# Performance work log

Hardware: AMD Instinct MI355X
Metric: run time of the kernel (lower is better)

## Reference

```python
import jax, jax.numpy as jnp
import numpy as np

DECAY = 0.99
EPS = 1e-12  # torch F.normalize eps


def setup_inputs() -> dict:
    key = jax.random.key(0)
    ks = jax.random.split(key, 5)
    B, S, H, M = 4, 4096, 1024, 256
    x = jax.random.normal(ks[0], (B, S, H), dtype=jnp.float32)
    Wq = jax.random.normal(ks[1], (M, H), dtype=jnp.float32) * (H ** -0.5)
    Wk = jax.random.normal(ks[2], (M, H), dtype=jnp.float32) * (H ** -0.5)
    Wv = jax.random.normal(ks[3], (M, H), dtype=jnp.float32) * (H ** -0.5)
    # original inits W_out to zeros; use small random weights so the baseline output is non-trivial
    Wo = jax.random.normal(ks[4], (H, M), dtype=jnp.float32) * (M ** -0.5)
    M0 = jnp.zeros((M, M), dtype=jnp.float32)
    return {"x": x, "Wq": Wq, "Wk": Wk, "Wv": Wv, "Wo": Wo, "M0": M0, "chunk_size": 64}


def _l2norm(t):
    return t / jnp.maximum(jnp.linalg.norm(t, axis=-1, keepdims=True), EPS)


def reference(x, Wq, Wk, Wv, Wo, M0, chunk_size):
    B, S, H = x.shape
    m = Wq.shape[0]
    q = jnp.einsum('bsh,mh->bsm', x, Wq)
    k = _l2norm(jnp.einsum('bsh,mh->bsm', x, Wk))
    v = _l2norm(jnp.einsum('bsh,mh->bsm', x, Wv))
    n_chunks = S // chunk_size
    # (n_chunks, B, c, m)
    qc = q.reshape(B, n_chunks, chunk_size, m).transpose(1, 0, 2, 3)
    kc = k.reshape(B, n_chunks, chunk_size, m).transpose(1, 0, 2, 3)
    vc = v.reshape(B, n_chunks, chunk_size, m).transpose(1, 0, 2, 3)
    decay_c = DECAY ** chunk_size
    scale = 1.0 / (B * chunk_size)

    def step(M, qkv):
        qch, kch, vch = qkv
        r = jnp.einsum('bcm,nm->bcn', qch, M)  # q @ M.T
        outer = jnp.einsum('bci,bcj->ij', vch, kch) * scale
        return decay_c * M + outer, r

    _, rs = jax.lax.scan(step, M0, (qc, kc, vc))  # rs: (n_chunks, B, c, m)
    retrieved = rs.transpose(1, 0, 2, 3).reshape(B, S, m)
    return jnp.einsum('bsm,hm->bsh', retrieved, Wo)
```

## Files before the change

### kernel.cpp

```cpp
#include <hip/hip_runtime.h>
#include <math.h>

#define BB 4
#define SS 4096
#define HH 1024
#define MM 256
#define CHUNK 64
#define NCHUNK 64
#define ROWS (BB*SS)
#define QKV_LD 768
#define DECAY_F 0.99

typedef unsigned short u16;
typedef __attribute__((ext_vector_type(8))) short bf16x8;
typedef __attribute__((ext_vector_type(8))) unsigned short u16x8;
typedef __attribute__((ext_vector_type(4))) float f32x4;

__device__ inline u16 f2b(float f) {
  union { float f; unsigned u; } v; v.f = f;
  unsigned r = v.u + 0x7FFF + ((v.u >> 16) & 1);
  return (u16)(r >> 16);
}
__device__ inline float b2f(u16 h) {
  union { unsigned u; float f; } v; v.u = ((unsigned)h) << 16; return v.f;
}

__device__ inline void gload16(const void* g, void* l) {
  __builtin_amdgcn_global_load_lds(
      (const __attribute__((address_space(1))) unsigned int*)g,
      (__attribute__((address_space(3))) unsigned int*)l, 16, 0, 0);
}

__global__ __launch_bounds__(256) void cast_x_kernel(const float* __restrict__ src,
                                                     u16* __restrict__ dst) {
  int i = blockIdx.x * 256 + threadIdx.x;
  float4 v = reinterpret_cast<const float4*>(src)[i];
  ushort4 o;
  o.x = f2b(v.x); o.y = f2b(v.y); o.z = f2b(v.z); o.w = f2b(v.w);
  reinterpret_cast<ushort4*>(dst)[i] = o;
}

__global__ __launch_bounds__(256) void cast_w_kernel(const float* __restrict__ Wq,
                                                     const float* __restrict__ Wk,
                                                     const float* __restrict__ Wv,
                                                     const float* __restrict__ Wo,
                                                     u16* __restrict__ Wqkv_b,
                                                     u16* __restrict__ Wo_b) {
  int b = blockIdx.x, which = b >> 8;
  int i = ((b & 255) << 8) + threadIdx.x;
  const float* src = which == 0 ? Wq : which == 1 ? Wk : which == 2 ? Wv : Wo;
  u16* dst = which < 3 ? Wqkv_b + which * (MM * HH) : Wo_b;
  float4 v = reinterpret_cast<const float4*>(src)[i];
  ushort4 o;
  o.x = f2b(v.x); o.y = f2b(v.y); o.z = f2b(v.z); o.w = f2b(v.w);
  reinterpret_cast<ushort4*>(dst)[i] = o;
}

template<int OUT_BF16>
__global__ __launch_bounds__(512, 2) void gemm256(const u16* __restrict__ A,
                                                  const u16* __restrict__ B,
                                                  void* __restrict__ Cv,
                                                  int K, int lda, int ldb, int ldc) {
  __shared__ bf16x8 LA[2][2][16][64];
  __shared__ bf16x8 LB[2][2][16][64];
  const int tid = threadIdx.x, lane = tid & 63, wv = tid >> 6;
  const int wr = wv >> 2, wc = wv & 3;

  const int gx = gridDim.x;
  const int nwg = gx * gridDim.y;
  const int lin = blockIdx.y * gx + blockIdx.x;
  const int chunk = nwg >> 3;
  const int orig = (lin & 7) * chunk + (lin >> 3);
  const int bx = orig % gx, by = orig / gx;
  const int row0 = by * 256, col0 = bx * 256;
  const int NT = K >> 6;

  const int fr = lane & 15;
  const int kg = (lane >> 4) << 3;

  auto stageA = [&](int kt, int db_, int tile) {
    const u16* g = A + (size_t)(row0 + tile * 16 + fr) * (size_t)lda + kt * 64 + kg;
    gload16(g,      &LA[db_][0][tile][0]);
    gload16(g + 32, &LA[db_][1][tile][0]);
  };
  auto stageB = [&](int kt, int db_, int tile) {
    const u16* g = B + (size_t)(col0 + tile * 16 + fr) * (size_t)ldb + kt * 64 + kg;
    gload16(g,      &LB[db_][0][tile][0]);
    gload16(g + 32, &LB[db_][1][tile][0]);
  };

  bf16x8 aq[4][2], bq[4][2];
  auto readAquad = [&](int db_, int h) {
#pragma unroll
    for (int i = 0; i < 4; ++i)
#pragma unroll
      for (int s = 0; s < 2; ++s)
        aq[i][s] = LA[db_][s][wr * 8 + h * 4 + i][lane];
  };
  auto readBall = [&](int db_) {
#pragma unroll
    for (int n = 0; n < 4; ++n)
#pragma unroll
      for (int s = 0; s < 2; ++s)
        bq[n][s] = LB[db_][s][wc * 4 + n][lane];
  };

  f32x4 acc[8][4] = {};
  auto cluster = [&](int h, int nh) {
#pragma unroll
    for (int i = 0; i < 4; ++i)
#pragma unroll
      for (int j = 0; j < 2; ++j)
#pragma unroll
        for (int s = 0; s < 2; ++s)
          acc[h * 4 + i][nh * 2 + j] = __builtin_amdgcn_mfma_f32_16x16x32_bf16(
              aq[i][s], bq[nh * 2 + j][s], acc[h * 4 + i][nh * 2 + j], 0, 0, 0);
  };

  stageA(0, 0, wv); stageA(0, 0, wv + 8);
  stageB(0, 0, wv); stageB(0, 0, wv + 8);

  for (int kt = 0; kt < NT; ++kt) {
    const int db = kt & 1, sb = db ^ 1;
    asm volatile("s_waitcnt vmcnt(0)" ::: "memory");
    __builtin_amdgcn_s_barrier();
    asm volatile("" ::: "memory");
    if (kt + 1 < NT) {
      stageA(kt + 1, sb, wv); stageA(kt + 1, sb, wv + 8);
      stageB(kt + 1, sb, wv); stageB(kt + 1, sb, wv + 8);
    }
    readAquad(db, 0);
    readBall(db);
    __builtin_amdgcn_s_setprio(1);
    cluster(0, 0); cluster(0, 1);
    __builtin_amdgcn_s_setprio(0);
    readAquad(db, 1);
    __builtin_amdgcn_s_setprio(1);
    cluster(1, 0); cluster(1, 1);
    __builtin_amdgcn_s_setprio(0);
  }

  const int r4 = (lane >> 4) << 2;
  const int cc = lane & 15;
#pragma unroll
  for (int mi = 0; mi < 8; ++mi)
#pragma unroll
    for (int nj = 0; nj < 4; ++nj)
#pragma unroll
      for (int r = 0; r < 4; ++r) {
        int lr = wr * 128 + mi * 16 + r4 + r;
        int lc = wc * 64 + nj * 16 + cc;
        float vv = acc[mi][nj][r];
        if (OUT_BF16) ((u16*)Cv)[(size_t)(row0 + lr) * ldc + col0 + lc] = f2b(vv);
        else          ((float*)Cv)[(size_t)(row0 + lr) * ldc + col0 + lc] = vv;
      }
}

#define M_OUTER 2
#define M_RETR  3

template<int MODE>
__global__ __launch_bounds__(256) void gemm128(const u16* __restrict__ A,
                                               const u16* __restrict__ Bg,
                                               void* __restrict__ Cv,
                                               int K, int lda, int ldb,
                                               float scale) {
  __shared__ bf16x8 As[3][512];
  __shared__ bf16x8 Bs[3][512];
  const int tid = threadIdx.x, lane = tid & 63, wv = tid >> 6;
  const int wr = wv >> 1, wc = wv & 1;
  const int t = blockIdx.z;
  const int bx = blockIdx.x, by = blockIdx.y;
  const int row0 = by * 128;
  const int col0 = bx * 128;
  const int NK = K >> 5;
  const u16* Bbase = (MODE == M_RETR) ? (Bg + (size_t)t * (MM * MM)) : Bg;

  auto stage = [&](int ks, int buf) {
    int koff;
    if (MODE == M_OUTER) koff = ((ks >> 1) << 12) + t * CHUNK + ((ks & 1) << 5);
    else                 koff = ks << 5;
#pragma unroll
    for (int j = 0; j < 2; ++j) {
      int m = j * 4 + wv;
      int rf = m * 16 + (lane & 15);
      size_t arow;
      if (MODE == M_RETR)
        arow = (size_t)(2 * by + (rf >> 6)) * SS + (size_t)t * CHUNK + (rf & 63);
      else
        arow = (size_t)(row0 + rf);
      const u16* ga = A + arow * (size_t)lda + koff + ((lane >> 4) << 3);
      gload16(ga, &As[buf][m * 64]);
      const u16* gb = Bbase + (size_t)(col0 + rf) * ldb + koff + ((lane >> 4) << 3);
      gload16(gb, &Bs[buf][m * 64]);
    }
  };

  f32x4 acc[4][4] = {};
  stage(0, 0);
  stage(1, 1);
  int rb = 0, sb = 2;
  for (int ks = 0; ks < NK; ++ks) {
    if (ks + 1 < NK) asm volatile("s_waitcnt vmcnt(4)" ::: "memory");
    else             asm volatile("s_waitcnt vmcnt(0)" ::: "memory");
    __builtin_amdgcn_s_barrier();
    asm volatile("" ::: "memory");
    if (ks + 2 < NK) stage(ks + 2, sb);
    bf16x8 af[4], bfr[4];
#pragma unroll
    for (int m = 0; m < 4; ++m) af[m] = As[rb][(wr * 4 + m) * 64 + lane];
#pragma unroll
    for (int n = 0; n < 4; ++n) bfr[n] = Bs[rb][(wc * 4 + n) * 64 + lane];
#pragma unroll
    for (int m = 0; m < 4; ++m)
#pragma unroll
      for (int n = 0; n < 4; ++n)
        acc[m][n] = __builtin_amdgcn_mfma_f32_16x16x32_bf16(af[m], bfr[n], acc[m][n], 0, 0, 0);
    rb = (rb == 2) ? 0 : rb + 1;
    sb = (sb == 2) ? 0 : sb + 1;
  }

  const int r4 = (lane >> 4) << 2;
  const int cc = lane & 15;
#pragma unroll
  for (int m = 0; m < 4; ++m)
#pragma unroll
    for (int n = 0; n < 4; ++n)
#pragma unroll
      for (int r = 0; r < 4; ++r) {
        int lr = wr * 64 + m * 16 + r4 + r;
        int lc = wc * 64 + n * 16 + cc;
        float vv = acc[m][n][r];
        if (MODE == M_OUTER) {
          ((float*)Cv)[(size_t)t * (MM * MM) + (size_t)(row0 + lr) * MM + col0 + lc] = vv * scale;
        } else {
          size_t rowg = (size_t)(2 * by + (lr >> 6)) * SS + (size_t)t * CHUNK + (lr & 63);
          ((u16*)Cv)[rowg * MM + col0 + lc] = f2b(vv);
        }
      }
}

__global__ __launch_bounds__(256) void l2normT_kernel(const u16* __restrict__ qkv,
                                                      u16* __restrict__ kT,
                                                      u16* __restrict__ vT) {
  __shared__ u16 T[256][72];
  __shared__ float ps[64][4];
  __shared__ float inv[64];
  const int tid = threadIdx.x;
  const int q = tid >> 6, rl = tid & 63;
  const int row0 = blockIdx.x * 64;
#pragma unroll 1
  for (int seg = 0; seg < 2; ++seg) {
    u16* dstT = seg ? vT : kT;
    const int segbase = 256 + seg * 256;
    float ss = 0.f;
#pragma unroll
    for (int i = 0; i < 8; ++i) {
      u16x8 v = *reinterpret_cast<const u16x8*>(
          qkv + (size_t)(row0 + rl) * QKV_LD + segbase + q * 64 + i * 8);
#pragma unroll
      for (int e = 0; e < 8; ++e) {
        float f = b2f(v[e]);
        ss += f * f;
        T[q * 64 + i * 8 + e][rl] = v[e];
      }
    }
    ps[rl][q] = ss;
    __syncthreads();
    if (tid < 64) {
      float s = ps[tid][0] + ps[tid][1] + ps[tid][2] + ps[tid][3];
      inv[tid] = 1.0f / fmaxf(sqrtf(s), 1e-12f);
    }
    __syncthreads();
#pragma unroll
    for (int p = 0; p < 8; ++p) {
      int c = p * 32 + q * 8 + (rl >> 3);
      int r0 = (rl & 7) * 8;
      u16x8 val = *reinterpret_cast<const u16x8*>(&T[c][r0]);
      u16x8 o;
#pragma unroll
      for (int e = 0; e < 8; ++e) o[e] = f2b(b2f(val[e]) * inv[r0 + e]);
      *reinterpret_cast<u16x8*>(dstT + (size_t)c * ROWS + row0 + r0) = o;
    }
    __syncthreads();
  }
}

__global__ __launch_bounds__(256) void prefix_kernel(const float* __restrict__ outer,
                                                     const float* __restrict__ M0,
                                                     u16* __restrict__ Mprev_b,
                                                     float decay_c) {
  int ij = blockIdx.x * 256 + threadIdx.x;
  float run = M0[ij];
  float pre[8];
#pragma unroll
  for (int d = 0; d < 8; ++d) pre[d] = outer[(size_t)d * (MM * MM) + ij];
#pragma unroll 1
  for (int tb = 0; tb < NCHUNK; tb += 8) {
#pragma unroll
    for (int d = 0; d < 8; ++d) {
      int tc = tb + d;
      float o = pre[d];
      if (tb + 8 < NCHUNK) pre[d] = outer[(size_t)(tc + 8) * (MM * MM) + ij];
      Mprev_b[(size_t)tc * (MM * MM) + ij] = f2b(run);
      run = decay_c * run + o;
    }
  }
}

extern "C" void kernel_launch(void* const* d_in, const int* in_sizes, int n_in,
                              void* d_out, int out_size, void* d_ws, size_t ws_size,
                              hipStream_t stream) {
  const float* x  = (const float*)d_in[0];
  const float* Wq = (const float*)d_in[1];
  const float* Wk = (const float*)d_in[2];
  const float* Wv = (const float*)d_in[3];
  const float* Wo = (const float*)d_in[4];
  const float* M0 = (const float*)d_in[5];
  float* out = (float*)d_out;

  char* ws = (char*)d_ws;
  u16*   xb      = (u16*)(ws);
  u16*   qkv_b   = (u16*)(ws + 33554432);
  u16*   Wqkv_b  = (u16*)(ws + 58720256);
  u16*   Wo_b    = (u16*)(ws + 60293120);
  u16*   kT      = (u16*)(ws);
  u16*   vT      = (u16*)(ws + 8388608);
  float* outer   = (float*)(ws + 16777216);
  u16*   Mprev_b = (u16*)(ws);
  u16*   r_b     = (u16*)(ws + 8388608);

  const float scale   = 1.0f / (BB * CHUNK);
  const float decay_c = (float)pow(DECAY_F, (double)CHUNK);
  dim3 blk(256), blk512(512);

  cast_x_kernel<<<(ROWS * HH / 4) / 256, blk, 0, stream>>>(x, xb);
  cast_w_kernel<<<1024, blk, 0, stream>>>(Wq, Wk, Wv, Wo, Wqkv_b, Wo_b);
  gemm256<1><<<dim3(QKV_LD / 256, ROWS / 256), blk512, 0, stream>>>(
      xb, Wqkv_b, qkv_b, HH, HH, HH, QKV_LD);
  l2normT_kernel<<<ROWS / 64, blk, 0, stream>>>(qkv_b, kT, vT);
  gemm128<M_OUTER><<<dim3(2, 2, NCHUNK), blk, 0, stream>>>(
      vT, kT, outer, MM, ROWS, ROWS, scale);
  prefix_kernel<<<(MM * MM) / 256, blk, 0, stream>>>(outer, M0, Mprev_b, decay_c);
  gemm128<M_RETR><<<dim3(2, 2, NCHUNK), blk, 0, stream>>>(
      qkv_b, Mprev_b, r_b, MM, QKV_LD, MM, 0.f);
  gemm256<0><<<dim3(HH / 256, ROWS / 256), blk512, 0, stream>>>(
      r_b, Wo_b, out, MM, MM, MM, HH);
}
```

Baseline: 151.1 us.

## Retile QKV GEMM to 256x192 tiles and interleave global prefetch with MFMA clusters

The gemm256 kernel gains an NBT template parameter. The QKV projection now uses 256x192 tiles, giving a 4x64 grid of 256 workgroups instead of 3x64 (192), so it fills the GPU's compute units better. The main loop no longer issues all next-tile global loads in one burst after the barrier. The loads are now spread across the four MFMA clusters, with partial vmcnt waits and extra barriers between phases, so memory traffic overlaps compute. The extra barriers add synchronisation cost and the 12-fragment layout gives an uneven B-tile split across waves.

```diff
diff --git a/kernel.cpp b/kernel.cpp
--- a/kernel.cpp
+++ b/kernel.cpp
@@ -56,15 +56,17 @@
   reinterpret_cast<ushort4*>(dst)[i] = o;
 }
 
-template<int OUT_BF16>
+template<int NBT, int OUT_BF16>
 __global__ __launch_bounds__(512, 2) void gemm256(const u16* __restrict__ A,
                                                   const u16* __restrict__ B,
                                                   void* __restrict__ Cv,
                                                   int K, int lda, int ldb, int ldc) {
+  constexpr int NFR = NBT / 4;
   __shared__ bf16x8 LA[2][2][16][64];
-  __shared__ bf16x8 LB[2][2][16][64];
+  __shared__ bf16x8 LB[2][2][NBT][64];
   const int tid = threadIdx.x, lane = tid & 63, wv = tid >> 6;
   const int wr = wv >> 2, wc = wv & 3;
+  const int ph3tile = (NBT == 16) ? (wv + 8) : (8 + (wv & 3));
 
   const int gx = gridDim.x;
   const int nwg = gx * gridDim.y;
@@ -72,7 +74,7 @@
   const int chunk = nwg >> 3;
   const int orig = (lin & 7) * chunk + (lin >> 3);
   const int bx = orig % gx, by = orig / gx;
-  const int row0 = by * 256, col0 = bx * 256;
+  const int row0 = by * 256, col0 = bx * (NBT * 16);
   const int NT = K >> 6;
 
   const int fr = lane & 15;
@@ -89,7 +91,7 @@
     gload16(g + 32, &LB[db_][1][tile][0]);
   };
 
-  bf16x8 aq[4][2], bq[4][2];
+  bf16x8 aq[4][2], bq[NFR][2];
   auto readAquad = [&](int db_, int h) {
 #pragma unroll
     for (int i = 0; i < 4; ++i)
@@ -97,47 +99,57 @@
       for (int s = 0; s < 2; ++s)
         aq[i][s] = LA[db_][s][wr * 8 + h * 4 + i][lane];
   };
-  auto readBall = [&](int db_) {
-#pragma unroll
-    for (int n = 0; n < 4; ++n)
+  auto readBhalf = [&](int db_, int half) {
+    const int n0 = half ? 2 : 0, n1 = half ? NFR : 2;
+#pragma unroll
+    for (int n = n0; n < n1; ++n)
 #pragma unroll
       for (int s = 0; s < 2; ++s)
-        bq[n][s] = LB[db_][s][wc * 4 + n][lane];
-  };
-
-  f32x4 acc[8][4] = {};
-  auto cluster = [&](int h, int nh) {
+        bq[n][s] = LB[db_][s][wc * NFR + n][lane];
+  };
+
+  f32x4 acc[8][NFR] = {};
+  auto cluster = [&](int h, int half) {
+    const int n0 = half ? 2 : 0, n1 = half ? NFR : 2;
 #pragma unroll
     for (int i = 0; i < 4; ++i)
 #pragma unroll
-      for (int j = 0; j < 2; ++j)
+      for (int n = n0; n < n1; ++n)
 #pragma unroll
         for (int s = 0; s < 2; ++s)
-          acc[h * 4 + i][nh * 2 + j] = __builtin_amdgcn_mfma_f32_16x16x32_bf16(
-              aq[i][s], bq[nh * 2 + j][s], acc[h * 4 + i][nh * 2 + j], 0, 0, 0);
+          acc[h * 4 + i][n] = __builtin_amdgcn_mfma_f32_16x16x32_bf16(
+              aq[i][s], bq[n][s], acc[h * 4 + i][n], 0, 0, 0);
   };
 
   stageA(0, 0, wv); stageA(0, 0, wv + 8);
-  stageB(0, 0, wv); stageB(0, 0, wv + 8);
+  stageB(0, 0, wv); stageB(0, 0, ph3tile);
 
   for (int kt = 0; kt < NT; ++kt) {
     const int db = kt & 1, sb = db ^ 1;
-    asm volatile("s_waitcnt vmcnt(0)" ::: "memory");
+    const bool pf = (kt + 1 < NT);
+    if (pf) stageA(kt + 1, sb, wv);
+    if (pf) asm volatile("s_waitcnt vmcnt(2)" ::: "memory");
+    else    asm volatile("s_waitcnt vmcnt(0)" ::: "memory");
     __builtin_amdgcn_s_barrier();
     asm volatile("" ::: "memory");
-    if (kt + 1 < NT) {
-      stageA(kt + 1, sb, wv); stageA(kt + 1, sb, wv + 8);
-      stageB(kt + 1, sb, wv); stageB(kt + 1, sb, wv + 8);
-    }
     readAquad(db, 0);
-    readBall(db);
-    __builtin_amdgcn_s_setprio(1);
-    cluster(0, 0); cluster(0, 1);
-    __builtin_amdgcn_s_setprio(0);
+    readBhalf(db, 0);
+    __builtin_amdgcn_s_setprio(1); cluster(0, 0); __builtin_amdgcn_s_setprio(0);
+    __builtin_amdgcn_s_barrier();
+    readBhalf(db, 1);
+    if (pf) stageA(kt + 1, sb, wv + 8);
+    __builtin_amdgcn_s_barrier();
+    __builtin_amdgcn_s_setprio(1); cluster(0, 1); __builtin_amdgcn_s_setprio(0);
+    __builtin_amdgcn_s_barrier();
     readAquad(db, 1);
-    __builtin_amdgcn_s_setprio(1);
-    cluster(1, 0); cluster(1, 1);
-    __builtin_amdgcn_s_setprio(0);
+    if (pf) stageB(kt + 1, sb, wv);
+    __builtin_amdgcn_s_barrier();
+    __builtin_amdgcn_s_setprio(1); cluster(1, 0); __builtin_amdgcn_s_setprio(0);
+    __builtin_amdgcn_s_barrier();
+    if (pf) stageB(kt + 1, sb, ph3tile);
+    __builtin_amdgcn_s_barrier();
+    __builtin_amdgcn_s_setprio(1); cluster(1, 1); __builtin_amdgcn_s_setprio(0);
+    __builtin_amdgcn_s_barrier();
   }
 
   const int r4 = (lane >> 4) << 2;
@@ -145,11 +157,11 @@
 #pragma unroll
   for (int mi = 0; mi < 8; ++mi)
 #pragma unroll
-    for (int nj = 0; nj < 4; ++nj)
+    for (int nj = 0; nj < NFR; ++nj)
 #pragma unroll
       for (int r = 0; r < 4; ++r) {
         int lr = wr * 128 + mi * 16 + r4 + r;
-        int lc = wc * 64 + nj * 16 + cc;
+        int lc = wc * (NFR * 16) + nj * 16 + cc;
         float vv = acc[mi][nj][r];
         if (OUT_BF16) ((u16*)Cv)[(size_t)(row0 + lr) * ldc + col0 + lc] = f2b(vv);
         else          ((float*)Cv)[(size_t)(row0 + lr) * ldc + col0 + lc] = vv;
@@ -336,7 +348,7 @@
 
   cast_x_kernel<<<(ROWS * HH / 4) / 256, blk, 0, stream>>>(x, xb);
   cast_w_kernel<<<1024, blk, 0, stream>>>(Wq, Wk, Wv, Wo, Wqkv_b, Wo_b);
-  gemm256<1><<<dim3(QKV_LD / 256, ROWS / 256), blk512, 0, stream>>>(
+  gemm256<12, 1><<<dim3(4, 64), blk512, 0, stream>>>(
       xb, Wqkv_b, qkv_b, HH, HH, HH, QKV_LD);
   l2normT_kernel<<<ROWS / 64, blk, 0, stream>>>(qkv_b, kT, vT);
   gemm128<M_OUTER><<<dim3(2, 2, NCHUNK), blk, 0, stream>>>(
@@ -344,6 +356,6 @@
   prefix_kernel<<<(MM * MM) / 256, blk, 0, stream>>>(outer, M0, Mprev_b, decay_c);
   gemm128<M_RETR><<<dim3(2, 2, NCHUNK), blk, 0, stream>>>(
       qkv_b, Mprev_b, r_b, MM, QKV_LD, MM, 0.f);
-  gemm256<0><<<dim3(HH / 256, ROWS / 256), blk512, 0, stream>>>(
+  gemm256<16, 0><<<dim3(4, 64), blk512, 0, stream>>>(
       r_b, Wo_b, out, MM, MM, MM, HH);
 }
```

New measurement: 146.4 us. -3.2%, faster.

## Shrink chunk GEMM tiles to 64x64, split l2norm by segment, interleave gemm256 prefetch

Applied to the files above, without the earlier changes.

Replaces the 128x128-tile outer-product and retrieval GEMMs with 64x64 tiles, taking the grid from 256 to 1024 blocks so the device's CUs have more work to spread across. The l2norm/transpose kernel now handles k and v in separate blocks through a second grid dimension instead of looping over both. The large gemm256 main loop issues its next-tile global loads in pieces between MFMA clusters, with extra barriers, rather than all at once after the wait. The cost is less reuse per block and added barrier overhead in gemm256.

```diff
diff --git a/kernel.cpp b/kernel.cpp
--- a/kernel.cpp
+++ b/kernel.cpp
@@ -97,12 +97,12 @@
       for (int s = 0; s < 2; ++s)
         aq[i][s] = LA[db_][s][wr * 8 + h * 4 + i][lane];
   };
-  auto readBall = [&](int db_) {
-#pragma unroll
-    for (int n = 0; n < 4; ++n)
+  auto readB2 = [&](int db_, int nh) {
+#pragma unroll
+    for (int j = 0; j < 2; ++j)
 #pragma unroll
       for (int s = 0; s < 2; ++s)
-        bq[n][s] = LB[db_][s][wc * 4 + n][lane];
+        bq[nh * 2 + j][s] = LB[db_][s][wc * 4 + nh * 2 + j][lane];
   };
 
   f32x4 acc[8][4] = {};
@@ -122,22 +122,30 @@
 
   for (int kt = 0; kt < NT; ++kt) {
     const int db = kt & 1, sb = db ^ 1;
-    asm volatile("s_waitcnt vmcnt(0)" ::: "memory");
+    const bool pf = (kt + 1 < NT);
+    if (pf) stageA(kt + 1, sb, wv);
+    if (pf) asm volatile("s_waitcnt vmcnt(2)" ::: "memory");
+    else    asm volatile("s_waitcnt vmcnt(0)" ::: "memory");
     __builtin_amdgcn_s_barrier();
     asm volatile("" ::: "memory");
-    if (kt + 1 < NT) {
-      stageA(kt + 1, sb, wv); stageA(kt + 1, sb, wv + 8);
-      stageB(kt + 1, sb, wv); stageB(kt + 1, sb, wv + 8);
-    }
     readAquad(db, 0);
-    readBall(db);
-    __builtin_amdgcn_s_setprio(1);
-    cluster(0, 0); cluster(0, 1);
-    __builtin_amdgcn_s_setprio(0);
+    readB2(db, 0);
+    __builtin_amdgcn_s_setprio(1); cluster(0, 0); __builtin_amdgcn_s_setprio(0);
+    __builtin_amdgcn_s_barrier();
+    readB2(db, 1);
+    if (pf) stageA(kt + 1, sb, wv + 8);
+    __builtin_amdgcn_s_barrier();
+    __builtin_amdgcn_s_setprio(1); cluster(0, 1); __builtin_amdgcn_s_setprio(0);
+    __builtin_amdgcn_s_barrier();
     readAquad(db, 1);
-    __builtin_amdgcn_s_setprio(1);
-    cluster(1, 0); cluster(1, 1);
-    __builtin_amdgcn_s_setprio(0);
+    if (pf) stageB(kt + 1, sb, wv);
+    __builtin_amdgcn_s_barrier();
+    __builtin_amdgcn_s_setprio(1); cluster(1, 0); __builtin_amdgcn_s_setprio(0);
+    __builtin_amdgcn_s_barrier();
+    if (pf) stageB(kt + 1, sb, wv + 8);
+    __builtin_amdgcn_s_barrier();
+    __builtin_amdgcn_s_setprio(1); cluster(1, 1); __builtin_amdgcn_s_setprio(0);
+    __builtin_amdgcn_s_barrier();
   }
 
   const int r4 = (lane >> 4) << 2;
@@ -156,66 +164,57 @@
       }
 }
 
-#define M_OUTER 2
-#define M_RETR  3
+#define G64_OUTER 0
+#define G64_RETR  1
 
 template<int MODE>
-__global__ __launch_bounds__(256) void gemm128(const u16* __restrict__ A,
-                                               const u16* __restrict__ Bg,
-                                               void* __restrict__ Cv,
-                                               int K, int lda, int ldb,
-                                               float scale) {
-  __shared__ bf16x8 As[3][512];
-  __shared__ bf16x8 Bs[3][512];
+__global__ __launch_bounds__(256) void gemm64(const u16* __restrict__ A,
+                                              const u16* __restrict__ Bg,
+                                              void* __restrict__ Cv,
+                                              float scale) {
+  __shared__ bf16x8 As[3][4][64];
+  __shared__ bf16x8 Bs[3][4][64];
+  constexpr int NK = 8;
   const int tid = threadIdx.x, lane = tid & 63, wv = tid >> 6;
   const int wr = wv >> 1, wc = wv & 1;
   const int t = blockIdx.z;
-  const int bx = blockIdx.x, by = blockIdx.y;
-  const int row0 = by * 128;
-  const int col0 = bx * 128;
-  const int NK = K >> 5;
-  const u16* Bbase = (MODE == M_RETR) ? (Bg + (size_t)t * (MM * MM)) : Bg;
+  const int i0 = blockIdx.y * 64;
+  const int j0 = blockIdx.x * 64;
+  const u16* Bbase = (MODE == G64_RETR) ? (Bg + (size_t)t * (MM * MM)) : Bg;
+  const int fr = lane & 15, kg = (lane >> 4) << 3;
 
   auto stage = [&](int ks, int buf) {
-    int koff;
-    if (MODE == M_OUTER) koff = ((ks >> 1) << 12) + t * CHUNK + ((ks & 1) << 5);
-    else                 koff = ks << 5;
-#pragma unroll
-    for (int j = 0; j < 2; ++j) {
-      int m = j * 4 + wv;
-      int rf = m * 16 + (lane & 15);
-      size_t arow;
-      if (MODE == M_RETR)
-        arow = (size_t)(2 * by + (rf >> 6)) * SS + (size_t)t * CHUNK + (rf & 63);
-      else
-        arow = (size_t)(row0 + rf);
-      const u16* ga = A + arow * (size_t)lda + koff + ((lane >> 4) << 3);
-      gload16(ga, &As[buf][m * 64]);
-      const u16* gb = Bbase + (size_t)(col0 + rf) * ldb + koff + ((lane >> 4) << 3);
-      gload16(gb, &Bs[buf][m * 64]);
+    if (MODE == G64_OUTER) {
+      int koff = ((ks >> 1) << 12) + t * CHUNK + ((ks & 1) << 5);
+      gload16(A     + (size_t)(i0 + wv * 16 + fr) * ROWS + koff + kg, &As[buf][wv][0]);
+      gload16(Bbase + (size_t)(j0 + wv * 16 + fr) * ROWS + koff + kg, &Bs[buf][wv][0]);
+    } else {
+      size_t arow = (size_t)blockIdx.y * SS + (size_t)t * CHUNK + wv * 16 + fr;
+      gload16(A     + arow * QKV_LD + ks * 32 + kg,                    &As[buf][wv][0]);
+      gload16(Bbase + (size_t)(j0 + wv * 16 + fr) * MM + ks * 32 + kg, &Bs[buf][wv][0]);
     }
   };
 
-  f32x4 acc[4][4] = {};
+  f32x4 acc[2][2] = {};
   stage(0, 0);
   stage(1, 1);
   int rb = 0, sb = 2;
   for (int ks = 0; ks < NK; ++ks) {
-    if (ks + 1 < NK) asm volatile("s_waitcnt vmcnt(4)" ::: "memory");
+    if (ks + 1 < NK) asm volatile("s_waitcnt vmcnt(2)" ::: "memory");
     else             asm volatile("s_waitcnt vmcnt(0)" ::: "memory");
     __builtin_amdgcn_s_barrier();
     asm volatile("" ::: "memory");
     if (ks + 2 < NK) stage(ks + 2, sb);
-    bf16x8 af[4], bfr[4];
-#pragma unroll
-    for (int m = 0; m < 4; ++m) af[m] = As[rb][(wr * 4 + m) * 64 + lane];
-#pragma unroll
-    for (int n = 0; n < 4; ++n) bfr[n] = Bs[rb][(wc * 4 + n) * 64 + lane];
-#pragma unroll
-    for (int m = 0; m < 4; ++m)
-#pragma unroll
-      for (int n = 0; n < 4; ++n)
-        acc[m][n] = __builtin_amdgcn_mfma_f32_16x16x32_bf16(af[m], bfr[n], acc[m][n], 0, 0, 0);
+    bf16x8 af[2], bf[2];
+#pragma unroll
+    for (int m = 0; m < 2; ++m) af[m] = As[rb][wr * 2 + m][lane];
+#pragma unroll
+    for (int n = 0; n < 2; ++n) bf[n] = Bs[rb][wc * 2 + n][lane];
+#pragma unroll
+    for (int m = 0; m < 2; ++m)
+#pragma unroll
+      for (int n = 0; n < 2; ++n)
+        acc[m][n] = __builtin_amdgcn_mfma_f32_16x16x32_bf16(af[m], bf[n], acc[m][n], 0, 0, 0);
     rb = (rb == 2) ? 0 : rb + 1;
     sb = (sb == 2) ? 0 : sb + 1;
   }
@@ -223,19 +222,19 @@
   const int r4 = (lane >> 4) << 2;
   const int cc = lane & 15;
 #pragma unroll
-  for (int m = 0; m < 4; ++m)
-#pragma unroll
-    for (int n = 0; n < 4; ++n)
+  for (int m = 0; m < 2; ++m)
+#pragma unroll
+    for (int n = 0; n < 2; ++n)
 #pragma unroll
       for (int r = 0; r < 4; ++r) {
-        int lr = wr * 64 + m * 16 + r4 + r;
-        int lc = wc * 64 + n * 16 + cc;
+        int lr = wr * 32 + m * 16 + r4 + r;
+        int lc = wc * 32 + n * 16 + cc;
         float vv = acc[m][n][r];
-        if (MODE == M_OUTER) {
-          ((float*)Cv)[(size_t)t * (MM * MM) + (size_t)(row0 + lr) * MM + col0 + lc] = vv * scale;
+        if (MODE == G64_OUTER) {
+          ((float*)Cv)[(size_t)t * (MM * MM) + (size_t)(i0 + lr) * MM + j0 + lc] = vv * scale;
         } else {
-          size_t rowg = (size_t)(2 * by + (lr >> 6)) * SS + (size_t)t * CHUNK + (lr & 63);
-          ((u16*)Cv)[rowg * MM + col0 + lc] = f2b(vv);
+          size_t rowg = (size_t)blockIdx.y * SS + (size_t)t * CHUNK + lr;
+          ((u16*)Cv)[rowg * MM + j0 + lc] = f2b(vv);
         }
       }
 }
@@ -249,40 +248,37 @@
   const int tid = threadIdx.x;
   const int q = tid >> 6, rl = tid & 63;
   const int row0 = blockIdx.x * 64;
-#pragma unroll 1
-  for (int seg = 0; seg < 2; ++seg) {
-    u16* dstT = seg ? vT : kT;
-    const int segbase = 256 + seg * 256;
-    float ss = 0.f;
-#pragma unroll
-    for (int i = 0; i < 8; ++i) {
-      u16x8 v = *reinterpret_cast<const u16x8*>(
-          qkv + (size_t)(row0 + rl) * QKV_LD + segbase + q * 64 + i * 8);
-#pragma unroll
-      for (int e = 0; e < 8; ++e) {
-        float f = b2f(v[e]);
-        ss += f * f;
-        T[q * 64 + i * 8 + e][rl] = v[e];
-      }
+  const int seg = blockIdx.y;
+  u16* dstT = seg ? vT : kT;
+  const int segbase = 256 + seg * 256;
+  float ss = 0.f;
+#pragma unroll
+  for (int i = 0; i < 8; ++i) {
+    u16x8 v = *reinterpret_cast<const u16x8*>(
+        qkv + (size_t)(row0 + rl) * QKV_LD + segbase + q * 64 + i * 8);
+#pragma unroll
+    for (int e = 0; e < 8; ++e) {
+      float f = b2f(v[e]);
+      ss += f * f;
+      T[q * 64 + i * 8 + e][rl] = v[e];
     }
-    ps[rl][q] = ss;
-    __syncthreads();
-    if (tid < 64) {
-      float s = ps[tid][0] + ps[tid][1] + ps[tid][2] + ps[tid][3];
-      inv[tid] = 1.0f / fmaxf(sqrtf(s), 1e-12f);
-    }
-    __syncthreads();
-#pragma unroll
-    for (int p = 0; p < 8; ++p) {
-      int c = p * 32 + q * 8 + (rl >> 3);
-      int r0 = (rl & 7) * 8;
-      u16x8 val = *reinterpret_cast<const u16x8*>(&T[c][r0]);
-      u16x8 o;
-#pragma unroll
-      for (int e = 0; e < 8; ++e) o[e] = f2b(b2f(val[e]) * inv[r0 + e]);
-      *reinterpret_cast<u16x8*>(dstT + (size_t)c * ROWS + row0 + r0) = o;
-    }
-    __syncthreads();
+  }
+  ps[rl][q] = ss;
+  __syncthreads();
+  if (tid < 64) {
+    float s = ps[tid][0] + ps[tid][1] + ps[tid][2] + ps[tid][3];
+    inv[tid] = 1.0f / fmaxf(sqrtf(s), 1e-12f);
+  }
+  __syncthreads();
+#pragma unroll
+  for (int p = 0; p < 8; ++p) {
+    int c = p * 32 + q * 8 + (rl >> 3);
+    int r0 = (rl & 7) * 8;
+    u16x8 val = *reinterpret_cast<const u16x8*>(&T[c][r0]);
+    u16x8 o;
+#pragma unroll
+    for (int e = 0; e < 8; ++e) o[e] = f2b(b2f(val[e]) * inv[r0 + e]);
+    *reinterpret_cast<u16x8*>(dstT + (size_t)c * ROWS + row0 + r0) = o;
   }
 }
 
@@ -338,12 +334,12 @@
   cast_w_kernel<<<1024, blk, 0, stream>>>(Wq, Wk, Wv, Wo, Wqkv_b, Wo_b);
   gemm256<1><<<dim3(QKV_LD / 256, ROWS / 256), blk512, 0, stream>>>(
       xb, Wqkv_b, qkv_b, HH, HH, HH, QKV_LD);
-  l2normT_kernel<<<ROWS / 64, blk, 0, stream>>>(qkv_b, kT, vT);
-  gemm128<M_OUTER><<<dim3(2, 2, NCHUNK), blk, 0, stream>>>(
-      vT, kT, outer, MM, ROWS, ROWS, scale);
+  l2normT_kernel<<<dim3(ROWS / 64, 2), blk, 0, stream>>>(qkv_b, kT, vT);
+  gemm64<G64_OUTER><<<dim3(4, 4, NCHUNK), blk, 0, stream>>>(
+      vT, kT, outer, scale);
   prefix_kernel<<<(MM * MM) / 256, blk, 0, stream>>>(outer, M0, Mprev_b, decay_c);
-  gemm128<M_RETR><<<dim3(2, 2, NCHUNK), blk, 0, stream>>>(
-      qkv_b, Mprev_b, r_b, MM, QKV_LD, MM, 0.f);
+  gemm64<G64_RETR><<<dim3(4, 4, NCHUNK), blk, 0, stream>>>(
+      qkv_b, Mprev_b, r_b, 0.f);
   gemm256<0><<<dim3(HH / 256, ROWS / 256), blk512, 0, stream>>>(
       r_b, Wo_b, out, MM, MM, MM, HH);
 }
```

After: 149.3 us. About the same (-1.2%).

## Fuse fp32-to-bf16 cast of x into QKV GEMM and interleave loads with MFMA

Applied to the files above, without the earlier changes.

Removes the standalone x cast kernel. The QKV GEMM now loads fp32 x into registers, converts it with v_cvt_pk_bf16_f32 and writes it to LDS itself. The main loop is also restructured so next-tile loads are spread between MFMA clusters, with partial vmcnt waits and extra barriers. This drops a full write and re-read of a 32MB bf16 copy of x, at the cost of reading fp32 x three times (once per column block), more registers and more barriers per iteration.

```diff
diff --git a/kernel.cpp b/kernel.cpp
--- a/kernel.cpp
+++ b/kernel.cpp
@@ -29,15 +29,6 @@
   __builtin_amdgcn_global_load_lds(
       (const __attribute__((address_space(1))) unsigned int*)g,
       (__attribute__((address_space(3))) unsigned int*)l, 16, 0, 0);
-}
-
-__global__ __launch_bounds__(256) void cast_x_kernel(const float* __restrict__ src,
-                                                     u16* __restrict__ dst) {
-  int i = blockIdx.x * 256 + threadIdx.x;
-  float4 v = reinterpret_cast<const float4*>(src)[i];
-  ushort4 o;
-  o.x = f2b(v.x); o.y = f2b(v.y); o.z = f2b(v.z); o.w = f2b(v.w);
-  reinterpret_cast<ushort4*>(dst)[i] = o;
 }
 
 __global__ __launch_bounds__(256) void cast_w_kernel(const float* __restrict__ Wq,
@@ -56,8 +47,8 @@
   reinterpret_cast<ushort4*>(dst)[i] = o;
 }
 
-template<int OUT_BF16>
-__global__ __launch_bounds__(512, 2) void gemm256(const u16* __restrict__ A,
+template<int A_F32, int OUT_BF16>
+__global__ __launch_bounds__(512, 2) void gemm256(const void* __restrict__ Ap,
                                                   const u16* __restrict__ B,
                                                   void* __restrict__ Cv,
                                                   int K, int lda, int ldb, int ldc) {
@@ -78,8 +69,39 @@
   const int fr = lane & 15;
   const int kg = (lane >> 4) << 3;
 
+  float4 rA[2][2][2];
+  auto loadA = [&](int kt) {
+    if constexpr (A_F32) {
+#pragma unroll
+      for (int j = 0; j < 2; ++j)
+#pragma unroll
+        for (int s = 0; s < 2; ++s) {
+          const float* g = (const float*)Ap +
+              (size_t)(row0 + (wv + j * 8) * 16 + fr) * (size_t)lda + kt * 64 + s * 32 + kg;
+          rA[j][s][0] = *(const float4*)g;
+          rA[j][s][1] = *(const float4*)(g + 4);
+        }
+    }
+  };
+  auto writeA = [&](int db_) {
+    if constexpr (A_F32) {
+#pragma unroll
+      for (int j = 0; j < 2; ++j)
+#pragma unroll
+        for (int s = 0; s < 2; ++s) {
+          float4 p = rA[j][s][0], q = rA[j][s][1];
+          unsigned w0, w1, w2, w3;
+          asm("v_cvt_pk_bf16_f32 %0, %1, %2" : "=v"(w0) : "v"(p.x), "v"(p.y));
+          asm("v_cvt_pk_bf16_f32 %0, %1, %2" : "=v"(w1) : "v"(p.z), "v"(p.w));
+          asm("v_cvt_pk_bf16_f32 %0, %1, %2" : "=v"(w2) : "v"(q.x), "v"(q.y));
+          asm("v_cvt_pk_bf16_f32 %0, %1, %2" : "=v"(w3) : "v"(q.z), "v"(q.w));
+          uint4 wd; wd.x = w0; wd.y = w1; wd.z = w2; wd.w = w3;
+          *reinterpret_cast<uint4*>(&LA[db_][s][wv + j * 8][lane]) = wd;
+        }
+    }
+  };
   auto stageA = [&](int kt, int db_, int tile) {
-    const u16* g = A + (size_t)(row0 + tile * 16 + fr) * (size_t)lda + kt * 64 + kg;
+    const u16* g = (const u16*)Ap + (size_t)(row0 + tile * 16 + fr) * (size_t)lda + kt * 64 + kg;
     gload16(g,      &LA[db_][0][tile][0]);
     gload16(g + 32, &LA[db_][1][tile][0]);
   };
@@ -97,12 +119,12 @@
       for (int s = 0; s < 2; ++s)
         aq[i][s] = LA[db_][s][wr * 8 + h * 4 + i][lane];
   };
-  auto readBall = [&](int db_) {
-#pragma unroll
-    for (int n = 0; n < 4; ++n)
+  auto readB2 = [&](int db_, int nh) {
+#pragma unroll
+    for (int j = 0; j < 2; ++j)
 #pragma unroll
       for (int s = 0; s < 2; ++s)
-        bq[n][s] = LB[db_][s][wc * 4 + n][lane];
+        bq[nh * 2 + j][s] = LB[db_][s][wc * 4 + nh * 2 + j][lane];
   };
 
   f32x4 acc[8][4] = {};
@@ -117,27 +139,44 @@
               aq[i][s], bq[nh * 2 + j][s], acc[h * 4 + i][nh * 2 + j], 0, 0, 0);
   };
 
-  stageA(0, 0, wv); stageA(0, 0, wv + 8);
-  stageB(0, 0, wv); stageB(0, 0, wv + 8);
+  if constexpr (A_F32) {
+    loadA(0);
+    stageB(0, 0, wv); stageB(0, 0, wv + 8);
+    writeA(0);
+  } else {
+    stageA(0, 0, wv); stageA(0, 0, wv + 8);
+    stageB(0, 0, wv); stageB(0, 0, wv + 8);
+  }
 
   for (int kt = 0; kt < NT; ++kt) {
     const int db = kt & 1, sb = db ^ 1;
-    asm volatile("s_waitcnt vmcnt(0)" ::: "memory");
+    const bool pf = (kt + 1 < NT);
+    if (pf) { if constexpr (A_F32) loadA(kt + 1); else stageA(kt + 1, sb, wv); }
+    if (pf) {
+      if constexpr (A_F32) asm volatile("s_waitcnt vmcnt(8)" ::: "memory");
+      else                 asm volatile("s_waitcnt vmcnt(2)" ::: "memory");
+    } else   asm volatile("s_waitcnt vmcnt(0)" ::: "memory");
+    if constexpr (A_F32) asm volatile("s_waitcnt lgkmcnt(0)" ::: "memory");
     __builtin_amdgcn_s_barrier();
     asm volatile("" ::: "memory");
-    if (kt + 1 < NT) {
-      stageA(kt + 1, sb, wv); stageA(kt + 1, sb, wv + 8);
-      stageB(kt + 1, sb, wv); stageB(kt + 1, sb, wv + 8);
-    }
     readAquad(db, 0);
-    readBall(db);
-    __builtin_amdgcn_s_setprio(1);
-    cluster(0, 0); cluster(0, 1);
-    __builtin_amdgcn_s_setprio(0);
+    readB2(db, 0);
+    __builtin_amdgcn_s_setprio(1); cluster(0, 0); __builtin_amdgcn_s_setprio(0);
+    __builtin_amdgcn_s_barrier();
+    readB2(db, 1);
+    if (pf) { if constexpr (A_F32) stageB(kt + 1, sb, wv); else stageA(kt + 1, sb, wv + 8); }
+    __builtin_amdgcn_s_barrier();
+    __builtin_amdgcn_s_setprio(1); cluster(0, 1); __builtin_amdgcn_s_setprio(0);
+    __builtin_amdgcn_s_barrier();
     readAquad(db, 1);
-    __builtin_amdgcn_s_setprio(1);
-    cluster(1, 0); cluster(1, 1);
-    __builtin_amdgcn_s_setprio(0);
+    if (pf) { if constexpr (A_F32) stageB(kt + 1, sb, wv + 8); else stageB(kt + 1, sb, wv); }
+    __builtin_amdgcn_s_barrier();
+    __builtin_amdgcn_s_setprio(1); cluster(1, 0); __builtin_amdgcn_s_setprio(0);
+    __builtin_amdgcn_s_barrier();
+    if (pf) { if constexpr (A_F32) writeA(sb); else stageB(kt + 1, sb, wv + 8); }
+    __builtin_amdgcn_s_barrier();
+    __builtin_amdgcn_s_setprio(1); cluster(1, 1); __builtin_amdgcn_s_setprio(0);
+    __builtin_amdgcn_s_barrier();
   }
 
   const int r4 = (lane >> 4) << 2;
@@ -320,7 +359,6 @@
   float* out = (float*)d_out;
 
   char* ws = (char*)d_ws;
-  u16*   xb      = (u16*)(ws);
   u16*   qkv_b   = (u16*)(ws + 33554432);
   u16*   Wqkv_b  = (u16*)(ws + 58720256);
   u16*   Wo_b    = (u16*)(ws + 60293120);
@@ -334,16 +372,15 @@
   const float decay_c = (float)pow(DECAY_F, (double)CHUNK);
   dim3 blk(256), blk512(512);
 
-  cast_x_kernel<<<(ROWS * HH / 4) / 256, blk, 0, stream>>>(x, xb);
   cast_w_kernel<<<1024, blk, 0, stream>>>(Wq, Wk, Wv, Wo, Wqkv_b, Wo_b);
-  gemm256<1><<<dim3(QKV_LD / 256, ROWS / 256), blk512, 0, stream>>>(
-      xb, Wqkv_b, qkv_b, HH, HH, HH, QKV_LD);
+  gemm256<1, 1><<<dim3(QKV_LD / 256, ROWS / 256), blk512, 0, stream>>>(
+      x, Wqkv_b, qkv_b, HH, HH, HH, QKV_LD);
   l2normT_kernel<<<ROWS / 64, blk, 0, stream>>>(qkv_b, kT, vT);
   gemm128<M_OUTER><<<dim3(2, 2, NCHUNK), blk, 0, stream>>>(
       vT, kT, outer, MM, ROWS, ROWS, scale);
   prefix_kernel<<<(MM * MM) / 256, blk, 0, stream>>>(outer, M0, Mprev_b, decay_c);
   gemm128<M_RETR><<<dim3(2, 2, NCHUNK), blk, 0, stream>>>(
       qkv_b, Mprev_b, r_b, MM, QKV_LD, MM, 0.f);
-  gemm256<0><<<dim3(HH / 256, ROWS / 256), blk512, 0, stream>>>(
+  gemm256<0, 0><<<dim3(HH / 256, ROWS / 256), blk512, 0, stream>>>(
       r_b, Wo_b, out, MM, MM, MM, HH);
 }
```

Measured after the change: 150.9 us. Within noise of the previous version (-0.2%).
